# Performance work log

Hardware: AMD Instinct MI355X
Metric: run time of the kernel (lower is better)

The kernel has to match this reference:

```python
import jax, jax.numpy as jnp
import numpy as np

D_MODEL = 1024
N_HEAD = 16


def setup_inputs() -> dict:
    key = jax.random.key(0)
    ks = jax.random.split(key, 11)
    B, S, D = 2, 2048, D_MODEL
    scale = 1.0 / np.sqrt(D)
    inp = {
        "query_tensor": jax.random.normal(ks[0], (B, S, D), jnp.float32),
        "key_tensor": jax.random.normal(ks[1], (B, S, D), jnp.float32),
        "value_tensor": jax.random.normal(ks[2], (B, S, D), jnp.float32),
        "w_q": jax.random.normal(ks[3], (D, D), jnp.float32) * scale,
        "b_q": jnp.zeros((D,), jnp.float32),
        "w_k": jax.random.normal(ks[4], (D, D), jnp.float32) * scale,
        "b_k": jnp.zeros((D,), jnp.float32),
        "w_v": jax.random.normal(ks[5], (D, D), jnp.float32) * scale,
        "b_v": jnp.zeros((D,), jnp.float32),
        "w_out": jax.random.normal(ks[6], (D, D), jnp.float32) * scale,
        "b_out": jnp.zeros((D,), jnp.float32),
    }
    return inp


def _split_heads(x, n_head):
    b, s, d = x.shape
    return x.reshape(b, s, n_head, d // n_head).transpose(0, 2, 1, 3)  # [b,h,s,dk]


def reference(query_tensor, key_tensor, value_tensor, w_q, b_q, w_k, b_k, w_v, b_v, w_out, b_out):
    # torch Linear: y = x @ W.T + b
    q = query_tensor @ w_q.T + b_q
    k = key_tensor @ w_k.T + b_k
    v = value_tensor @ w_v.T + b_v
    q = _split_heads(q, N_HEAD)
    k = _split_heads(k, N_HEAD)
    v = _split_heads(v, N_HEAD)
    d_k = k.shape[-1]
    scores = jnp.einsum("bhqd,bhkd->bhqk", q, k) / jnp.sqrt(jnp.float32(d_k))
    attn = jax.nn.softmax(scores, axis=-1)
    ctx = jnp.einsum("bhqk,bhkd->bhqd", attn, v)
    b, h, s, dk = ctx.shape
    ctx = ctx.transpose(0, 2, 1, 3).reshape(b, s, h * dk)
    return ctx @ w_out.T + b_out
```

## Files before the change

### kernel.cpp

```cpp
#include <hip/hip_runtime.h>
#include <hip/hip_bf16.h>

using ushort = unsigned short;

typedef __attribute__((ext_vector_type(8))) short bf16x8;
typedef __attribute__((ext_vector_type(4))) float f32x4;
typedef __attribute__((ext_vector_type(16))) float f32x16;
typedef __attribute__((ext_vector_type(4))) unsigned short u16x4;

#define DEVINL __device__ __forceinline__


static constexpr size_t WQ_O = 12582912;
static constexpr size_t WO_O = 15728640;
static constexpr size_t QB_O = 16777216;
static constexpr size_t KB_O = 20971520;
static constexpr size_t VT_O = 25165824;
static constexpr size_t CTX_O = 0;

DEVINL ushort f2bf(float f) {
  unsigned u = __builtin_bit_cast(unsigned, f);
  u += 0x7fffu + ((u >> 16) & 1u);
  return (ushort)(u >> 16);
}

DEVINL void gld16(const ushort* g, ushort* lds) {
  __builtin_amdgcn_global_load_lds(
      (const __attribute__((address_space(1))) void*)g,
      (__attribute__((address_space(3))) void*)lds, 16, 0, 0);
}

__global__ __launch_bounds__(256) void cvt_w(
    const float* __restrict__ wq, const float* __restrict__ wk,
    const float* __restrict__ wv, const float* __restrict__ wo,
    ushort* __restrict__ ws)
{
  int e = (blockIdx.x * 256 + threadIdx.x) * 8;
  const float* s;
  if      (e < 1048576) s = wq + e;
  else if (e < 2097152) s = wk + (e - 1048576);
  else if (e < 3145728) s = wv + (e - 2097152);
  else                  s = wo + (e - 3145728);
  float4 a = *(const float4*)s;
  float4 b = *(const float4*)(s + 4);
  union { u16x4 v; ushort u[4]; } r0, r1;
  r0.u[0] = f2bf(a.x); r0.u[1] = f2bf(a.y); r0.u[2] = f2bf(a.z); r0.u[3] = f2bf(a.w);
  r1.u[0] = f2bf(b.x); r1.u[1] = f2bf(b.y); r1.u[2] = f2bf(b.z); r1.u[3] = f2bf(b.w);
  *(u16x4*)(ws + WQ_O + e) = r0.v;
  *(u16x4*)(ws + WQ_O + e + 4) = r1.v;
}

template<bool CVTA>
DEVINL void gemm_core(const void* __restrict__ Av, const ushort* __restrict__ Bw,
                      const float* __restrict__ bias, void* __restrict__ Cout,
                      float scale, int omode, int row0, int col0)
{
  constexpr int K = 1024;
  __shared__ ushort As[128 * 64];
  __shared__ ushort Bs[128 * 64];
  const int t = threadIdx.x;
  const int l = t & 63;
  const int w = t >> 6;
  const int wr = w >> 1, wc = w & 1;

  const int srow = t >> 3;
  const int scol8 = (t & 7) * 8;
  const int swz_half = ((((t & 7) * 16) ^ ((srow & 7) << 4)) >> 1);

  const ushort* Ap16 = (const ushort*)Av + (size_t)(row0 + srow) * K + scol8;
  const float*  Ap32 = (const float*)Av + (size_t)(row0 + srow) * K + scol8;
  const ushort* Bp = Bw + (size_t)(col0 + srow) * K + scol8;

  bf16x8 areg[4], breg[4];
  float4 a32[4][2];
  auto loadstage = [&](int k0) {
#pragma unroll
    for (int i = 0; i < 4; ++i) {
      if constexpr (CVTA) {
        a32[i][0] = *(const float4*)(Ap32 + (size_t)(i * 32) * K + k0);
        a32[i][1] = *(const float4*)(Ap32 + (size_t)(i * 32) * K + k0 + 4);
      } else {
        areg[i] = *(const bf16x8*)(Ap16 + (size_t)(i * 32) * K + k0);
      }
      breg[i] = *(const bf16x8*)(Bp + (size_t)(i * 32) * K + k0);
    }
  };

  f32x4 acc[4][4];
#pragma unroll
  for (int i = 0; i < 4; ++i)
#pragma unroll
    for (int j = 0; j < 4; ++j) acc[i][j] = (f32x4){0.f, 0.f, 0.f, 0.f};

  loadstage(0);
#pragma unroll 1
  for (int kt = 0; kt < K / 64; ++kt) {
    __syncthreads();
#pragma unroll
    for (int i = 0; i < 4; ++i) {
      if constexpr (CVTA) {
        union { bf16x8 v; unsigned u[4]; } pk;
        asm("v_cvt_pk_bf16_f32 %0, %1, %2" : "=v"(pk.u[0]) : "v"(a32[i][0].x), "v"(a32[i][0].y));
        asm("v_cvt_pk_bf16_f32 %0, %1, %2" : "=v"(pk.u[1]) : "v"(a32[i][0].z), "v"(a32[i][0].w));
        asm("v_cvt_pk_bf16_f32 %0, %1, %2" : "=v"(pk.u[2]) : "v"(a32[i][1].x), "v"(a32[i][1].y));
        asm("v_cvt_pk_bf16_f32 %0, %1, %2" : "=v"(pk.u[3]) : "v"(a32[i][1].z), "v"(a32[i][1].w));
        *(bf16x8*)&As[(srow + i * 32) * 64 + swz_half] = pk.v;
      } else {
        *(bf16x8*)&As[(srow + i * 32) * 64 + swz_half] = areg[i];
      }
      *(bf16x8*)&Bs[(srow + i * 32) * 64 + swz_half] = breg[i];
    }
    if (kt + 1 < K / 64) loadstage((kt + 1) * 64);
    __syncthreads();
#pragma unroll
    for (int ks = 0; ks < 2; ++ks) {
      bf16x8 af[4], bfr[4];
#pragma unroll
      for (int mi = 0; mi < 4; ++mi) {
        int r = wr * 64 + mi * 16 + (l & 15);
        int cb = ((ks << 6) | ((l >> 4) << 4)) ^ ((r & 7) << 4);
        af[mi] = *(const bf16x8*)&As[r * 64 + (cb >> 1)];
      }
#pragma unroll
      for (int nj = 0; nj < 4; ++nj) {
        int r = wc * 64 + nj * 16 + (l & 15);
        int cb = ((ks << 6) | ((l >> 4) << 4)) ^ ((r & 7) << 4);
        bfr[nj] = *(const bf16x8*)&Bs[r * 64 + (cb >> 1)];
      }
#pragma unroll
      for (int mi = 0; mi < 4; ++mi)
#pragma unroll
        for (int nj = 0; nj < 4; ++nj)
          acc[mi][nj] = __builtin_amdgcn_mfma_f32_16x16x32_bf16(af[mi], bfr[nj], acc[mi][nj], 0, 0, 0);
    }
  }

  const int cl = l & 15;
#pragma unroll
  for (int mi = 0; mi < 4; ++mi) {
#pragma unroll
    for (int nj = 0; nj < 4; ++nj) {
      int n = col0 + wc * 64 + nj * 16 + cl;
      float bv = bias[n];
      int mbase = row0 + wr * 64 + mi * 16 + (l >> 4) * 4;
      if (omode == 1) {
        float* Of = (float*)Cout;
#pragma unroll
        for (int ri = 0; ri < 4; ++ri)
          Of[(size_t)(mbase + ri) * 1024 + n] = (acc[mi][nj][ri] + bv) * scale;
      } else if (omode == 0) {
        ushort* Ob = (ushort*)Cout;
        int h = n >> 6, d = n & 63;
#pragma unroll
        for (int ri = 0; ri < 4; ++ri) {
          int m = mbase + ri;
          int b = m >> 11, s = m & 2047;
          Ob[(size_t)((b * 16 + h) * 2048 + s) * 64 + d] = f2bf((acc[mi][nj][ri] + bv) * scale);
        }
      } else {
        ushort* Ob = (ushort*)Cout;
        int h = n >> 6, d = n & 63;
        int b = mbase >> 11, s = mbase & 2047;
        union { u16x4 v; ushort u[4]; } pk;
#pragma unroll
        for (int ri = 0; ri < 4; ++ri) pk.u[ri] = f2bf((acc[mi][nj][ri] + bv) * scale);
        *(u16x4*)&Ob[(size_t)((b * 16 + h) * 64 + d) * 2048 + s] = pk.v;
      }
    }
  }
}

__global__ __launch_bounds__(256, 2) void gemm_qkv(
    const float* __restrict__ xq, const float* __restrict__ xk, const float* __restrict__ xv,
    const ushort* __restrict__ ws_c, ushort* __restrict__ ws_m,
    const float* __restrict__ bq, const float* __restrict__ bk, const float* __restrict__ bv)
{
  int lin = blockIdx.z * 256 + blockIdx.y * 8 + blockIdx.x;
  int swz = (lin & 7) * 96 + (lin >> 3);
  int z = swz >> 8, rem = swz & 255;
  int by = rem >> 3, bx = rem & 7;
  const float* A = (z == 0) ? xq : ((z == 1) ? xk : xv);
  const ushort* W = ws_c + WQ_O + (size_t)z * 1048576;
  const float* bias = (z == 0) ? bq : ((z == 1) ? bk : bv);
  ushort* dst = ws_m + QB_O + (size_t)z * 4194304;
  float scale = (z == 0) ? (0.125f * 1.4426950408889634f) : 1.0f;
  int omode = (z == 2) ? 2 : 0;
  gemm_core<true>(A, W, bias, dst, scale, omode, by * 128, bx * 128);
}

__global__ __launch_bounds__(256, 2) void gemm_out(
    const ushort* __restrict__ ctx, const ushort* __restrict__ wo,
    const float* __restrict__ bo, float* __restrict__ out)
{
  int lin = blockIdx.y * 8 + blockIdx.x;
  int swz = (lin & 7) * 32 + (lin >> 3);
  int by = swz >> 3, bx = swz & 7;
  gemm_core<false>(ctx, wo, bo, out, 1.0f, 1, by * 128, bx * 128);
}

__global__ __launch_bounds__(512, 4) void attn8(
    const ushort* __restrict__ Qb, const ushort* __restrict__ Kb,
    const ushort* __restrict__ Vtb, ushort* __restrict__ Ctx)
{
  __shared__ ushort smem[32768];

  const int t = threadIdx.x, l = t & 63, w = t >> 6;
  const int wq4 = w & 3, half = w >> 2;
  const int hi2 = l >> 5, q = l & 31;
  const int bh = blockIdx.y, qt = blockIdx.x;
  const int kvb = half * 1024;
  const ushort* Qp = Qb + ((size_t)bh * 2048 + qt * 128 + wq4 * 32) * 64;
  const ushort* Kp = Kb + (size_t)bh * 2048 * 64;
  const ushort* Vp = Vtb + (size_t)bh * 64 * 2048;

  ushort* Ksh = smem + half * 8192;
  ushort* Vsh = smem + 16384 + half * 8192;

  bf16x8 qf[4];
#pragma unroll
  for (int ks = 0; ks < 4; ++ks)
    qf[ks] = *(const bf16x8*)(Qp + q * 64 + ks * 16 + hi2 * 8);

  auto stageKV = [&](int pp, int kv0) {
#pragma unroll
    for (int i = 0; i < 2; ++i) {
      int R = (i * 4 + wq4) * 8 + (l >> 3);
      int g = l & 7;
      int sR = (R & ~12) | ((R & 4) << 1) | ((R & 8) >> 1);
      gld16(Kp + (size_t)(kv0 + sR) * 64 + (g ^ (R & 7)) * 8,
            Ksh + pp * 4096 + (i * 4 + wq4) * 512);
      gld16(Vp + (size_t)R * 2048 + kv0 + (g ^ (R & 7)) * 8,
            Vsh + pp * 4096 + (i * 4 + wq4) * 512);
    }
  };

  f32x16 acc0, acc1;
#pragma unroll
  for (int i = 0; i < 16; ++i) { acc0[i] = 0.f; acc1[i] = 0.f; }
  f32x16 Zv;
#pragma unroll
  for (int i = 0; i < 16; ++i) Zv[i] = 0.f;
  float lrun = 0.f;

  const int rsw = (q & 7) << 4;

  stageKV(0, kvb);
  __syncthreads();

#pragma unroll 1
  for (int kt = 0; kt < 16; ++kt) {
    const int p = kt & 1;
    const ushort* Kl = Ksh + p * 4096;
    const ushort* Vl = Vsh + p * 4096;

    f32x16 scA, scB;
    __builtin_amdgcn_s_setprio(1);
    {
      bf16x8 kf = *(const bf16x8*)&Kl[q * 64 + (((hi2 * 16)) ^ rsw) / 2];
      scA = __builtin_amdgcn_mfma_f32_32x32x16_bf16(kf, qf[0], Zv, 0, 0, 0);
#pragma unroll
      for (int ks = 1; ks < 4; ++ks) {
        bf16x8 k2 = *(const bf16x8*)&Kl[q * 64 + (((ks * 32 + hi2 * 16) ^ rsw) >> 1)];
        scA = __builtin_amdgcn_mfma_f32_32x32x16_bf16(k2, qf[ks], scA, 0, 0, 0);
      }
      const int r1 = (32 + q) * 64;
      bf16x8 kg = *(const bf16x8*)&Kl[r1 + (((hi2 * 16)) ^ rsw) / 2];
      scB = __builtin_amdgcn_mfma_f32_32x32x16_bf16(kg, qf[0], Zv, 0, 0, 0);
#pragma unroll
      for (int ks = 1; ks < 4; ++ks) {
        bf16x8 k2 = *(const bf16x8*)&Kl[r1 + (((ks * 32 + hi2 * 16) ^ rsw) >> 1)];
        scB = __builtin_amdgcn_mfma_f32_32x32x16_bf16(k2, qf[ks], scB, 0, 0, 0);
      }
    }
    __builtin_amdgcn_s_setprio(0);

    if (kt + 1 < 16) stageKV(p ^ 1, kvb + (kt + 1) * 64);

#pragma unroll
    for (int c = 0; c < 2; ++c) {
      f32x16& sc = (c == 0) ? scA : scB;
      float s0 = 0.f, s1 = 0.f, s2 = 0.f, s3 = 0.f;
#pragma unroll
      for (int i = 0; i < 4; ++i) {
        float e0 = __builtin_amdgcn_exp2f(sc[i]);      sc[i] = e0;      s0 += e0;
        float e1 = __builtin_amdgcn_exp2f(sc[4 + i]);  sc[4 + i] = e1;  s1 += e1;
        float e2 = __builtin_amdgcn_exp2f(sc[8 + i]);  sc[8 + i] = e2;  s2 += e2;
        float e3 = __builtin_amdgcn_exp2f(sc[12 + i]); sc[12 + i] = e3; s3 += e3;
      }
      lrun += (s0 + s1) + (s2 + s3);

      union PU { bf16x8 v; unsigned u[4]; } pA, pB;
#pragma unroll
      for (int i = 0; i < 4; ++i) {
        asm("v_cvt_pk_bf16_f32 %0, %1, %2" : "=v"(pA.u[i]) : "v"(sc[2 * i]), "v"(sc[2 * i + 1]));
        asm("v_cvt_pk_bf16_f32 %0, %1, %2" : "=v"(pB.u[i]) : "v"(sc[8 + 2 * i]), "v"(sc[9 + 2 * i]));
      }

      __builtin_amdgcn_s_setprio(1);
#pragma unroll
      for (int db = 0; db < 2; ++db) {
        const int d = db * 32 + q;
        bf16x8 va = *(const bf16x8*)&Vl[d * 64 + (((c * 64 + hi2 * 16) ^ rsw) >> 1)];
        bf16x8 vb = *(const bf16x8*)&Vl[d * 64 + (((c * 64 + 32 + hi2 * 16) ^ rsw) >> 1)];
        if (db == 0) {
          acc0 = __builtin_amdgcn_mfma_f32_32x32x16_bf16(va, pA.v, acc0, 0, 0, 0);
          acc0 = __builtin_amdgcn_mfma_f32_32x32x16_bf16(vb, pB.v, acc0, 0, 0, 0);
        } else {
          acc1 = __builtin_amdgcn_mfma_f32_32x32x16_bf16(va, pA.v, acc1, 0, 0, 0);
          acc1 = __builtin_amdgcn_mfma_f32_32x32x16_bf16(vb, pB.v, acc1, 0, 0, 0);
        }
      }
      __builtin_amdgcn_s_setprio(0);
    }
    __syncthreads();
  }

  float lsum = lrun + __shfl_xor(lrun, 32);
  float* Lf = (float*)smem;

  if (l < 32) Lf[half * 128 + wq4 * 32 + q] = lsum;
  __syncthreads();
  const float inv = 1.0f / (Lf[wq4 * 32 + q] + Lf[128 + wq4 * 32 + q]);
  __syncthreads();

  if (half == 1) {
    float* base = Lf + (wq4 * 32 + q) * 64;
#pragma unroll
    for (int db = 0; db < 2; ++db)
#pragma unroll
      for (int g = 0; g < 4; ++g) {
        float4 v;
        if (db == 0) v = (float4){acc0[g * 4], acc0[g * 4 + 1], acc0[g * 4 + 2], acc0[g * 4 + 3]};
        else         v = (float4){acc1[g * 4], acc1[g * 4 + 1], acc1[g * 4 + 2], acc1[g * 4 + 3]};
        *(float4*)(base + db * 32 + g * 8 + hi2 * 4) = v;
      }
  }
  __syncthreads();

  if (half == 0) {
    float* base = Lf + (wq4 * 32 + q) * 64;
#pragma unroll
    for (int db = 0; db < 2; ++db)
#pragma unroll
      for (int g = 0; g < 4; ++g) {
        float* p = base + db * 32 + g * 8 + hi2 * 4;
        float4 pv = *(float4*)p;
        float4 o;
        if (db == 0) o = (float4){(acc0[g * 4] + pv.x) * inv, (acc0[g * 4 + 1] + pv.y) * inv,
                                  (acc0[g * 4 + 2] + pv.z) * inv, (acc0[g * 4 + 3] + pv.w) * inv};
        else         o = (float4){(acc1[g * 4] + pv.x) * inv, (acc1[g * 4 + 1] + pv.y) * inv,
                                  (acc1[g * 4 + 2] + pv.z) * inv, (acc1[g * 4 + 3] + pv.w) * inv};
        *(float4*)p = o;
      }
  }
  __syncthreads();

  {
    const int b = bh >> 4, h = bh & 15;
    const int d0 = (l & 7) * 8;
#pragma unroll
    for (int rr = 0; rr < 2; ++rr) {
      int row = w * 16 + rr * 8 + (l >> 3);
      float4 f0 = *(const float4*)(Lf + row * 64 + d0);
      float4 f1 = *(const float4*)(Lf + row * 64 + d0 + 4);
      union { u16x4 v; ushort u[4]; } o0, o1;
      o0.u[0] = f2bf(f0.x); o0.u[1] = f2bf(f0.y); o0.u[2] = f2bf(f0.z); o0.u[3] = f2bf(f0.w);
      o1.u[0] = f2bf(f1.x); o1.u[1] = f2bf(f1.y); o1.u[2] = f2bf(f1.z); o1.u[3] = f2bf(f1.w);
      ushort* dst = Ctx + ((size_t)b * 2048 + qt * 128 + row) * 1024 + h * 64 + d0;
      *(u16x4*)dst = o0.v;
      *(u16x4*)(dst + 4) = o1.v;
    }
  }
}

extern "C" void kernel_launch(void* const* d_in, const int* in_sizes, int n_in,
                              void* d_out, int out_size, void* d_ws, size_t ws_size,
                              hipStream_t stream) {
  const float* xq = (const float*)d_in[0];
  const float* xk = (const float*)d_in[1];
  const float* xv = (const float*)d_in[2];
  const float* wq = (const float*)d_in[3];
  const float* bq = (const float*)d_in[4];
  const float* wk = (const float*)d_in[5];
  const float* bk = (const float*)d_in[6];
  const float* wv = (const float*)d_in[7];
  const float* bv = (const float*)d_in[8];
  const float* wo = (const float*)d_in[9];
  const float* bo = (const float*)d_in[10];
  ushort* ws = (ushort*)d_ws;

  cvt_w<<<2048, 256, 0, stream>>>(wq, wk, wv, wo, ws);
  gemm_qkv<<<dim3(8, 32, 3), 256, 0, stream>>>(xq, xk, xv, ws, ws, bq, bk, bv);
  attn8<<<dim3(16, 32), 512, 0, stream>>>(ws + QB_O, ws + KB_O, ws + VT_O, ws + CTX_O);
  gemm_out<<<dim3(8, 32), 256, 0, stream>>>(ws + CTX_O, ws + WO_O, bo, (float*)d_out);
}
```

Measured before the change: 108.8 us.

## Use 128x64 tiles for output GEMM, remap block order, swizzle attention merge LDS

The GEMM core is templated on tile width, so the output projection can use 128x64 tiles. That doubles its grid to 512 blocks to fill more CUs. The QKV GEMM and attention kernels get new block-index-to-tile mappings aimed at XCD-aware L2 locality. The attention epilogue's shared-memory merge buffer gets an XOR swizzle to reduce LDS bank conflicts. In exchange, the narrower output tiles give less reuse of each A tile and issue more loads per MFMA.

```diff
diff --git a/kernel.cpp b/kernel.cpp
--- a/kernel.cpp
+++ b/kernel.cpp
@@ -50,14 +50,16 @@
   *(u16x4*)(ws + WQ_O + e + 4) = r1.v;
 }
 
-template<bool CVTA>
+template<bool CVTA, int BN>
 DEVINL void gemm_core(const void* __restrict__ Av, const ushort* __restrict__ Bw,
                       const float* __restrict__ bias, void* __restrict__ Cout,
                       float scale, int omode, int row0, int col0)
 {
   constexpr int K = 1024;
+  constexpr int BI = BN / 32;
+  constexpr int NJ = BN / 32;
   __shared__ ushort As[128 * 64];
-  __shared__ ushort Bs[128 * 64];
+  __shared__ ushort Bs[BN * 64];
   const int t = threadIdx.x;
   const int l = t & 63;
   const int w = t >> 6;
@@ -71,7 +73,7 @@
   const float*  Ap32 = (const float*)Av + (size_t)(row0 + srow) * K + scol8;
   const ushort* Bp = Bw + (size_t)(col0 + srow) * K + scol8;
 
-  bf16x8 areg[4], breg[4];
+  bf16x8 areg[4], breg[BI];
   float4 a32[4][2];
   auto loadstage = [&](int k0) {
 #pragma unroll
@@ -82,15 +84,17 @@
       } else {
         areg[i] = *(const bf16x8*)(Ap16 + (size_t)(i * 32) * K + k0);
       }
+    }
+#pragma unroll
+    for (int i = 0; i < BI; ++i)
       breg[i] = *(const bf16x8*)(Bp + (size_t)(i * 32) * K + k0);
-    }
   };
 
-  f32x4 acc[4][4];
+  f32x4 acc[4][NJ];
 #pragma unroll
   for (int i = 0; i < 4; ++i)
 #pragma unroll
-    for (int j = 0; j < 4; ++j) acc[i][j] = (f32x4){0.f, 0.f, 0.f, 0.f};
+    for (int j = 0; j < NJ; ++j) acc[i][j] = (f32x4){0.f, 0.f, 0.f, 0.f};
 
   loadstage(0);
 #pragma unroll 1
@@ -108,13 +112,15 @@
       } else {
         *(bf16x8*)&As[(srow + i * 32) * 64 + swz_half] = areg[i];
       }
+    }
+#pragma unroll
+    for (int i = 0; i < BI; ++i)
       *(bf16x8*)&Bs[(srow + i * 32) * 64 + swz_half] = breg[i];
-    }
     if (kt + 1 < K / 64) loadstage((kt + 1) * 64);
     __syncthreads();
 #pragma unroll
     for (int ks = 0; ks < 2; ++ks) {
-      bf16x8 af[4], bfr[4];
+      bf16x8 af[4], bfr[NJ];
 #pragma unroll
       for (int mi = 0; mi < 4; ++mi) {
         int r = wr * 64 + mi * 16 + (l & 15);
@@ -122,15 +128,15 @@
         af[mi] = *(const bf16x8*)&As[r * 64 + (cb >> 1)];
       }
 #pragma unroll
-      for (int nj = 0; nj < 4; ++nj) {
-        int r = wc * 64 + nj * 16 + (l & 15);
+      for (int nj = 0; nj < NJ; ++nj) {
+        int r = wc * (BN / 2) + nj * 16 + (l & 15);
         int cb = ((ks << 6) | ((l >> 4) << 4)) ^ ((r & 7) << 4);
         bfr[nj] = *(const bf16x8*)&Bs[r * 64 + (cb >> 1)];
       }
 #pragma unroll
       for (int mi = 0; mi < 4; ++mi)
 #pragma unroll
-        for (int nj = 0; nj < 4; ++nj)
+        for (int nj = 0; nj < NJ; ++nj)
           acc[mi][nj] = __builtin_amdgcn_mfma_f32_16x16x32_bf16(af[mi], bfr[nj], acc[mi][nj], 0, 0, 0);
     }
   }
@@ -139,8 +145,8 @@
 #pragma unroll
   for (int mi = 0; mi < 4; ++mi) {
 #pragma unroll
-    for (int nj = 0; nj < 4; ++nj) {
-      int n = col0 + wc * 64 + nj * 16 + cl;
+    for (int nj = 0; nj < NJ; ++nj) {
+      int n = col0 + wc * (BN / 2) + nj * 16 + cl;
       float bv = bias[n];
       int mbase = row0 + wr * 64 + mi * 16 + (l >> 4) * 4;
       if (omode == 1) {
@@ -175,27 +181,26 @@
     const ushort* __restrict__ ws_c, ushort* __restrict__ ws_m,
     const float* __restrict__ bq, const float* __restrict__ bk, const float* __restrict__ bv)
 {
-  int lin = blockIdx.z * 256 + blockIdx.y * 8 + blockIdx.x;
-  int swz = (lin & 7) * 96 + (lin >> 3);
-  int z = swz >> 8, rem = swz & 255;
-  int by = rem >> 3, bx = rem & 7;
+  const int hw = blockIdx.x + 8 * blockIdx.y + 256 * blockIdx.z;
+  const int X = hw & 7, j = hw >> 3;
+  const int g = 8 * (j >> 3) + X;
+  const int bx = j & 7;
+  const int by = g & 31, z = g >> 5;
+
   const float* A = (z == 0) ? xq : ((z == 1) ? xk : xv);
   const ushort* W = ws_c + WQ_O + (size_t)z * 1048576;
   const float* bias = (z == 0) ? bq : ((z == 1) ? bk : bv);
   ushort* dst = ws_m + QB_O + (size_t)z * 4194304;
   float scale = (z == 0) ? (0.125f * 1.4426950408889634f) : 1.0f;
   int omode = (z == 2) ? 2 : 0;
-  gemm_core<true>(A, W, bias, dst, scale, omode, by * 128, bx * 128);
+  gemm_core<true, 128>(A, W, bias, dst, scale, omode, by * 128, bx * 128);
 }
 
 __global__ __launch_bounds__(256, 2) void gemm_out(
     const ushort* __restrict__ ctx, const ushort* __restrict__ wo,
     const float* __restrict__ bo, float* __restrict__ out)
 {
-  int lin = blockIdx.y * 8 + blockIdx.x;
-  int swz = (lin & 7) * 32 + (lin >> 3);
-  int by = swz >> 3, bx = swz & 7;
-  gemm_core<false>(ctx, wo, bo, out, 1.0f, 1, by * 128, bx * 128);
+  gemm_core<false, 64>(ctx, wo, bo, out, 1.0f, 1, blockIdx.y * 128, blockIdx.x * 64);
 }
 
 __global__ __launch_bounds__(512, 4) void attn8(
@@ -207,7 +212,12 @@
   const int t = threadIdx.x, l = t & 63, w = t >> 6;
   const int wq4 = w & 3, half = w >> 2;
   const int hi2 = l >> 5, q = l & 31;
-  const int bh = blockIdx.y, qt = blockIdx.x;
+
+  const int hw = blockIdx.y * 16 + blockIdx.x;
+  const int j = hw >> 3;
+  const int bh = (hw & 7) + 8 * (j >> 4);
+  const int qt = j & 15;
+
   const int kvb = half * 1024;
   const ushort* Qp = Qb + ((size_t)bh * 2048 + qt * 128 + wq4 * 32) * 64;
   const ushort* Kp = Kb + (size_t)bh * 2048 * 64;
@@ -323,8 +333,12 @@
   const float inv = 1.0f / (Lf[wq4 * 32 + q] + Lf[128 + wq4 * 32 + q]);
   __syncthreads();
 
+  auto mrg = [&](int row, int G) -> float* {
+    return Lf + row * 64 + ((G ^ (row & 15)) << 2);
+  };
+
   if (half == 1) {
-    float* base = Lf + (wq4 * 32 + q) * 64;
+    const int row = wq4 * 32 + q;
 #pragma unroll
     for (int db = 0; db < 2; ++db)
 #pragma unroll
@@ -332,18 +346,18 @@
         float4 v;
         if (db == 0) v = (float4){acc0[g * 4], acc0[g * 4 + 1], acc0[g * 4 + 2], acc0[g * 4 + 3]};
         else         v = (float4){acc1[g * 4], acc1[g * 4 + 1], acc1[g * 4 + 2], acc1[g * 4 + 3]};
-        *(float4*)(base + db * 32 + g * 8 + hi2 * 4) = v;
+        *(float4*)mrg(row, db * 8 + g * 2 + hi2) = v;
       }
   }
   __syncthreads();
 
   if (half == 0) {
-    float* base = Lf + (wq4 * 32 + q) * 64;
+    const int row = wq4 * 32 + q;
 #pragma unroll
     for (int db = 0; db < 2; ++db)
 #pragma unroll
       for (int g = 0; g < 4; ++g) {
-        float* p = base + db * 32 + g * 8 + hi2 * 4;
+        float* p = mrg(row, db * 8 + g * 2 + hi2);
         float4 pv = *(float4*)p;
         float4 o;
         if (db == 0) o = (float4){(acc0[g * 4] + pv.x) * inv, (acc0[g * 4 + 1] + pv.y) * inv,
@@ -361,8 +375,8 @@
 #pragma unroll
     for (int rr = 0; rr < 2; ++rr) {
       int row = w * 16 + rr * 8 + (l >> 3);
-      float4 f0 = *(const float4*)(Lf + row * 64 + d0);
-      float4 f1 = *(const float4*)(Lf + row * 64 + d0 + 4);
+      float4 f0 = *(const float4*)mrg(row, (l & 7) * 2);
+      float4 f1 = *(const float4*)mrg(row, (l & 7) * 2 + 1);
       union { u16x4 v; ushort u[4]; } o0, o1;
       o0.u[0] = f2bf(f0.x); o0.u[1] = f2bf(f0.y); o0.u[2] = f2bf(f0.z); o0.u[3] = f2bf(f0.w);
       o1.u[0] = f2bf(f1.x); o1.u[1] = f2bf(f1.y); o1.u[2] = f2bf(f1.z); o1.u[3] = f2bf(f1.w);
@@ -392,5 +406,5 @@
   cvt_w<<<2048, 256, 0, stream>>>(wq, wk, wv, wo, ws);
   gemm_qkv<<<dim3(8, 32, 3), 256, 0, stream>>>(xq, xk, xv, ws, ws, bq, bk, bv);
   attn8<<<dim3(16, 32), 512, 0, stream>>>(ws + QB_O, ws + KB_O, ws + VT_O, ws + CTX_O);
-  gemm_out<<<dim3(8, 32), 256, 0, stream>>>(ws + CTX_O, ws + WO_O, bo, (float*)d_out);
-}
+  gemm_out<<<dim3(16, 32), 256, 0, stream>>>(ws + CTX_O, ws + WO_O, bo, (float*)d_out);
+}
```

After: 103.9 us. -4.5%, faster.
